# Kernel tuning notes

Hardware: AMD Instinct MI355X
Metric: run time of the kernel (lower is better)

Reference implementation:

```python
import jax, jax.numpy as jnp
import numpy as np

FRAME = 512
HOP = 256
FS = 16000
XI_H1 = 31.622776601683793
P_H0 = 0.5
P_H1 = 0.5
SMOOTH_T = 0.072
ALPHA = float(np.exp(-HOP / (FS * SMOOTH_T)))  # time_to_smoothing_constant
EPS = float(np.finfo(np.float32).eps)


def _sqrt_hann():
    # periodic Hann (torch.hann_window default), then sqrt (sqrt=True in STFTTorch)
    n = np.arange(FRAME)
    w = 0.5 * (1.0 - np.cos(2.0 * np.pi * n / FRAME))
    return jnp.asarray(np.sqrt(w), dtype=jnp.float32)


def _stft_power(x):
    # x: [B, N] time signal -> [B, F, T] power spectrogram (|STFT|^2)
    pad = FRAME // 2
    xp = jnp.pad(x, ((0, 0), (pad, pad)), mode='reflect')  # center=True, reflect
    T = (xp.shape[1] - FRAME) // HOP + 1
    idx = jnp.arange(T)[:, None] * HOP + jnp.arange(FRAME)[None, :]
    frames = xp[:, idx] * _sqrt_hann()          # [B, T, FRAME]
    spec = jnp.fft.rfft(frames, axis=-1)        # [B, T, F], F = FRAME//2 + 1
    power = spec.real ** 2 + spec.imag ** 2
    return jnp.transpose(power, (0, 2, 1)).astype(jnp.float32)  # [B, F, T]


def setup_inputs() -> dict:
    key = jax.random.key(0)
    k1, k2, k3 = jax.random.split(key, 3)
    B, N = 64, 128000
    F, T = FRAME // 2 + 1, N // HOP + 1  # 257, 501
    return {
        'spp_estimate': jax.random.uniform(k1, (B, 1, F, T), dtype=jnp.float32),
        'input_sig': jax.random.normal(k2, (B, 1, N), dtype=jnp.float32),
        'interference': jax.random.normal(k3, (B, 1, N), dtype=jnp.float32),
    }


def reference(spp_estimate, input_sig, interference):
    noise_p = _stft_power(interference[:, 0])   # [B, F, T]
    noisy_p = _stft_power(input_sig[:, 0])      # [B, F, T]

    # EMA noise-variance recursion over frames (sequential dependency)
    p = jnp.transpose(noise_p, (2, 0, 1))       # [T, B, F]

    def step(v, pt):
        v2 = ALPHA * v + (1.0 - ALPHA) * pt
        return v2, v2

    v0 = p[0]
    _, vs = jax.lax.scan(step, v0, p[1:])
    var_noise = jnp.concatenate([v0[None], vs], axis=0)  # [T, B, F]
    var_noise = jnp.transpose(var_noise, (1, 2, 0))      # [B, F, T]

    # a-posteriori SPP
    ratio = (P_H0 / P_H1) * (1.0 + XI_H1)
    expo = -noisy_p / (var_noise + EPS) * (XI_H1 / (1.0 + XI_H1))
    spp_oracle = 1.0 / (1.0 + ratio * jnp.exp(expo))

    est = spp_estimate[:, 0]                    # [B, F, T]
    loss = jnp.mean((est - spp_oracle) ** 2)
    return loss
```

## Files before the change

### kernel.cpp

```cpp
#include <hip/hip_runtime.h>
#include <hip/hip_bf16.h>
#include <math.h>

typedef __attribute__((ext_vector_type(8))) short bf16x8;
typedef __attribute__((ext_vector_type(4))) float f32x4;
typedef __attribute__((ext_vector_type(8))) _Float16 h8;
typedef unsigned long long u64;

#define NSAMP  128000
#define TFR    501
#define TP     512
#define FPOW   257
#define NF     257
#define B_SZ   64
#define CHUNKT 32
#define NCH    16
#define EPS_F  1.1920928955078125e-07f

#define SEG    16640
#define ASEGB  66560
#define BPHB   32768

__global__ __launch_bounds__(256)
void build_basis(unsigned short* __restrict__ Bt) {
    int col = blockIdx.x;
    int g = col >> 5, o = col & 15;
    int isIm = (col >> 4) & 1;
    int bin = g * 16 + o;
    for (int k = threadIdx.x; k < 512; k += 256) {
        float w = sinf((float)k * (float)(M_PI / 512.0));
        float v;
        if (col == 16) {
            v = w * ((k & 1) ? -1.f : 1.f);
        } else {
            int mm = (bin * k) & 511;
            float th = (float)mm * (float)(2.0 * M_PI / 512.0);
            v = w * (isIm ? -sinf(th) : cosf(th));
        }
        __hip_bfloat16 h = __float2bfloat16(v);
        int ph = k >> 5, kq = (k >> 3) & 3, j = k & 7;
        size_t idx = (((size_t)ph * 32 + (col >> 4)) * 64
                      + kq * 16 + (col & 15)) * 8 + j;
        Bt[idx] = *reinterpret_cast<unsigned short*>(&h);
    }
}

__global__ __launch_bounds__(512)
void dft_gemm(const float* __restrict__ sig,
              const float* __restrict__ intf,
              const unsigned short* __restrict__ Bt,
              _Float16* __restrict__ powo)
{
    extern __shared__ char As[];

    const int mchunk = blockIdx.x, b = blockIdx.y, s = blockIdx.z;
    const int tid = threadIdx.x, lane = tid & 63, wn = tid >> 6;
    const int lq = lane >> 4, ll = lane & 15;
    const float* x = (s == 0 ? intf : sig) + (size_t)b * NSAMP;
    const int tbase = mchunk * 16384 - 256;

    if (mchunk >= 1 && mchunk <= 6) {
        const char* xg = (const char*)(x + tbase);
        #pragma unroll
        for (int r = 0; r < 8; ++r) {
            int o = r * 8192 + tid * 16;
            __builtin_amdgcn_global_load_lds(
                (const __attribute__((address_space(1))) void*)(xg + o),
                (__attribute__((address_space(3))) void*)(As + o), 16, 0, 0);
        }
        if (tid < 64) {
            int o = 65536 + tid * 16;
            __builtin_amdgcn_global_load_lds(
                (const __attribute__((address_space(1))) void*)(xg + o),
                (__attribute__((address_space(3))) void*)(As + o), 16, 0, 0);
        }
    } else if (mchunk == 0) {
        const char* xg = (const char*)x;
        #pragma unroll
        for (int r = 0; r < 8; ++r) {
            int o = 1024 + r * 8192 + tid * 16;
            __builtin_amdgcn_global_load_lds(
                (const __attribute__((address_space(1))) void*)(xg + o - 1024),
                (__attribute__((address_space(3))) void*)(As + o), 16, 0, 0);
        }
    } else {
        const char* xg = (const char*)(x + tbase);
        #pragma unroll
        for (int r = 0; r < 6; ++r) {
            int o = r * 8192 + tid * 16;
            __builtin_amdgcn_global_load_lds(
                (const __attribute__((address_space(1))) void*)(xg + o),
                (__attribute__((address_space(3))) void*)(As + o), 16, 0, 0);
        }
        if (tid < 320) {
            int o = 49152 + tid * 16;
            __builtin_amdgcn_global_load_lds(
                (const __attribute__((address_space(1))) void*)(xg + o),
                (__attribute__((address_space(3))) void*)(As + o), 16, 0, 0);
        }
    }

    const char* bb = (const char*)Bt + (size_t)(wn * 4 * 64 + lane) * 16;
    bf16x8 B0[4], B1[4];
    auto loadPh = [&](int ph, bf16x8 (&dst)[4]) {
        const char* bp = bb + (size_t)ph * BPHB;
        #pragma unroll
        for (int nf = 0; nf < 4; ++nf)
            dst[nf] = *(const bf16x8*)(bp + nf * 1024);
    };
    loadPh(0, B0);

    asm volatile("s_waitcnt vmcnt(0)" ::: "memory");
    __syncthreads();

    if (mchunk == 0) {
        if (tid < 256) {
            float v = *(const float*)(As + (512 - tid) * 4);
            *(float*)(As + tid * 4) = v;
        }
        __syncthreads();
    } else if (mchunk == 7) {
        #pragma unroll
        for (int q = 0; q < 6; ++q) {
            int j = 13568 + q * 512 + tid;
            float v = *(const float*)(As + (27134 - j) * 4);
            *(float*)(As + j * 4) = v;
        }
        __syncthreads();
    }

    {
        float fr[32];
        float fx[4];
        #pragma unroll
        for (int q = 0; q < 8; ++q) {
            f32x4 v = *(const f32x4*)(As + (q * 512 + tid) * 16);
            fr[q*4+0] = v[0]; fr[q*4+1] = v[1];
            fr[q*4+2] = v[2]; fr[q*4+3] = v[3];
        }
        if (tid < 64) {
            f32x4 v = *(const f32x4*)(As + (4096 + tid) * 16);
            fx[0] = v[0]; fx[1] = v[1]; fx[2] = v[2]; fx[3] = v[3];
        }
        __syncthreads();
        #pragma unroll
        for (int q = 0; q < 8; ++q) {
            unsigned short h[4];
            #pragma unroll
            for (int e = 0; e < 4; ++e) {
                __hip_bfloat16 t = __float2bfloat16(fr[q*4+e]);
                h[e] = *(unsigned short*)&t;
            }
            int a = (q * 512 + tid) * 8;
            a ^= ((a >> 9) & 7) << 4;
            *(u64*)(As + a) = (u64)h[0] | ((u64)h[1] << 16) |
                              ((u64)h[2] << 32) | ((u64)h[3] << 48);
        }
        if (tid < 64) {
            unsigned short h[4];
            #pragma unroll
            for (int e = 0; e < 4; ++e) {
                __hip_bfloat16 t = __float2bfloat16(fx[e]);
                h[e] = *(unsigned short*)&t;
            }
            int a = (4096 + tid) * 8;
            *(u64*)(As + a) = (u64)h[0] | ((u64)h[1] << 16) |
                              ((u64)h[2] << 32) | ((u64)h[3] << 48);
        }
        __syncthreads();
    }

    f32x4 acc[4][4];
    #pragma unroll
    for (int i = 0; i < 4; ++i)
        #pragma unroll
        for (int j = 0; j < 4; ++j) acc[i][j] = 0;

    auto doPhase = [&](int ph, bf16x8 (&cur)[4]) {
        bf16x8 af[4];
        #pragma unroll
        for (int mf = 0; mf < 4; ++mf) {
            int a = (mf * 16 + ll) * 512 + ph * 64 + lq * 16;
            a ^= ((a >> 9) & 7) << 4;
            af[mf] = *(const bf16x8*)(As + a);
        }
        __builtin_amdgcn_s_setprio(1);
        #pragma unroll
        for (int mf = 0; mf < 4; ++mf)
            #pragma unroll
            for (int nf = 0; nf < 4; ++nf)
                acc[mf][nf] = __builtin_amdgcn_mfma_f32_16x16x32_bf16(
                    af[mf], cur[nf], acc[mf][nf], 0, 0, 0);
        __builtin_amdgcn_s_setprio(0);
    };

    #pragma unroll 1
    for (int pp2 = 0; pp2 < 8; ++pp2) {
        const int ph = pp2 * 2;
        loadPh(ph + 1, B1);
        doPhase(ph, B0);
        if (pp2 < 7) loadPh(ph + 2, B0);
        doPhase(ph + 1, B1);
    }

    const int sb = s * 64 + b;
    _Float16* pbase = powo + (size_t)sb * FPOW * TP;
    #pragma unroll
    for (int mf = 0; mf < 4; ++mf) {
        const int rl0 = mchunk * 64 + mf * 16 + lq * 4;
        #pragma unroll
        for (int p = 0; p < 2; ++p) {
            f32x4 re = acc[mf][2 * p], im = acc[mf][2 * p + 1];
            int gbin = wn * 2 + p;
            int bin = gbin * 16 + ll;
            bool nyq = (gbin == 0) && (ll == 0);
            unsigned short hp[4], hn[4];
            #pragma unroll
            for (int j = 0; j < 4; ++j) {
                float pr = re[j] * re[j];
                float pi = im[j] * im[j];
                _Float16 hv = (_Float16)(nyq ? pr : (pr + pi));
                hp[j] = *(unsigned short*)&hv;
                _Float16 hw = (_Float16)pi;
                hn[j] = *(unsigned short*)&hw;
            }
            u64 pk = (u64)hp[0] | ((u64)hp[1] << 16) |
                     ((u64)hp[2] << 32) | ((u64)hp[3] << 48);
            *(u64*)(pbase + (size_t)bin * TP + rl0) = pk;
            if (nyq) {
                u64 pk2 = (u64)hn[0] | ((u64)hn[1] << 16) |
                          ((u64)hn[2] << 32) | ((u64)hn[3] << 48);
                *(u64*)(pbase + (size_t)256 * TP + rl0) = pk2;
            }
        }
    }
}

template<int W>
__device__ __forceinline__ float warm_fixed(const _Float16* __restrict__ nrow,
                                            int base, float alpha, float oma) {
    h8 blk[W / 8];
    #pragma unroll
    for (int i = 0; i < W / 8; ++i)
        blk[i] = *(const h8*)(nrow + base + i * 8);
    float v = (float)blk[0][0];
    #pragma unroll
    for (int i = 1; i < W; ++i)
        v = fmaf(alpha, v, oma * (float)blk[i / 8][i % 8]);
    v = fmaf(alpha, v, oma * (float)nrow[base + W]);
    return v;
}

__global__ __launch_bounds__(256, 4)
void spp_loss_kernel(const _Float16* __restrict__ noiseP,
                     const _Float16* __restrict__ noisyP,
                     const float* __restrict__ est,
                     float* __restrict__ out,
                     float alpha)
{
    const double XI = 31.622776601683793;
    const float RATIO = (float)(1.0 + XI);
    const float COEF  = (float)(XI / (1.0 + XI));
    const float INVN  = (float)(1.0 / ((double)B_SZ * NF * TFR));

    int tid = blockIdx.x * blockDim.x + threadIdx.x;
    int f   = tid % NF;
    int rem = tid / NF;
    int c   = rem & (NCH - 1);
    int b   = rem >> 4;

    float local = 0.f;
    if (b < B_SZ) {
        const int t0   = c * CHUNKT;
        const int tend = min(TFR, t0 + CHUNKT);
        const _Float16* nrow = noiseP + ((size_t)b * NF + f) * TP;
        const _Float16* yrow = noisyP + ((size_t)b * NF + f) * TP;
        const float* erow = est + ((size_t)b * NF + f) * TFR;
        const float oma = 1.f - alpha;

        float v;
        if (t0 == 0)            v = (float)nrow[0];
        else if (t0 == CHUNKT)  v = warm_fixed<32>(nrow, 0, alpha, oma);
        else                    v = warm_fixed<48>(nrow, t0 - 48, alpha, oma);

        h8 wn8[4], wy8[4];
        #pragma unroll
        for (int i = 0; i < 4; ++i) {
            wn8[i] = *(const h8*)(nrow + t0 + i * 8);
            wy8[i] = *(const h8*)(yrow + t0 + i * 8);
        }
        float last_n = (float)nrow[t0 + 32];
        float last_y = (float)yrow[t0 + 32];
        float qe[32];
        #pragma unroll
        for (int i = 0; i < 32; ++i)
            qe[i] = erow[min(t0 + 1 + i, TFR - 1)];

        {
            float np = (float)wy8[0][0];
            float e0 = erow[t0];
            float expo = -np / (v + EPS_F) * COEF;
            float spp  = 1.f / fmaf(RATIO, __expf(expo), 1.f);
            float d = e0 - spp;
            local = fmaf(d, d, local);
        }
        #pragma unroll
        for (int i = 0; i < 32; ++i) {
            int t = t0 + 1 + i;
            float nv = (i < 31) ? (float)wn8[(i + 1) / 8][(i + 1) % 8] : last_n;
            v = fmaf(alpha, v, oma * nv);
            if (t < tend) {
                float yv = (i < 31) ? (float)wy8[(i + 1) / 8][(i + 1) % 8] : last_y;
                float expo = -yv / (v + EPS_F) * COEF;
                float spp  = 1.f / fmaf(RATIO, __expf(expo), 1.f);
                float d = qe[i] - spp;
                local = fmaf(d, d, local);
            }
        }
    }

    for (int off = 32; off > 0; off >>= 1)
        local += __shfl_down(local, off);
    __shared__ float wsum[4];
    if ((threadIdx.x & 63) == 0) wsum[threadIdx.x >> 6] = local;
    __syncthreads();
    if (threadIdx.x == 0) {
        float ssum = (wsum[0] + wsum[1]) + (wsum[2] + wsum[3]);
        atomicAdd(out, ssum * INVN);
    }
}

extern "C" void kernel_launch(void* const* d_in, const int* in_sizes, int n_in,
                              void* d_out, int out_size, void* d_ws, size_t ws_size,
                              hipStream_t stream) {
    const float* est  = (const float*)d_in[0];
    const float* sig  = (const float*)d_in[1];
    const float* intf = (const float*)d_in[2];

    unsigned short* Bt = (unsigned short*)d_ws;
    _Float16* powp = (_Float16*)((char*)d_ws + (size_t)512 * 1024);

    hipLaunchKernelGGL(build_basis, dim3(512), dim3(256), 0, stream, Bt);
    hipMemsetAsync(d_out, 0, sizeof(float), stream);

    hipFuncSetAttribute((const void*)dft_gemm,
                        hipFuncAttributeMaxDynamicSharedMemorySize, ASEGB);
    dim3 gG(8, 64, 2);
    hipLaunchKernelGGL(dft_gemm, gG, dim3(512), ASEGB, stream,
                       sig, intf, Bt, powp);

    const double alpha_d = exp(-((double)256) / (16000.0 * 0.072));
    const _Float16* noiseP = powp;
    const _Float16* noisyP = powp + (size_t)B_SZ * FPOW * TP;
    dim3 gB((B_SZ * NCH * NF + 255) / 256);
    hipLaunchKernelGGL(spp_loss_kernel, gB, dim3(256), 0, stream,
                       noiseP, noisyP, est, (float*)d_out, (float)alpha_d);
}
```

Measured before the change: 84.98 us.

## Split DFT into even/odd bins via folded windowed frames to halve GEMM K

Applies the sqrt-Hann window in the kernel and folds each 512-sample frame into sum and difference halves (x[m]±x[m+256]). Even bins then come from the sum half and odd bins from the difference half, so each wave group runs a K=256 GEMM instead of K=512. The basis is rebuilt as two 256-row groups, and a window table is staged in LDS. This halves the MFMA work and basis traffic, at the cost of extra LDS and some pre-processing arithmetic.

```diff
diff --git a/kernel.cpp b/kernel.cpp
--- a/kernel.cpp
+++ b/kernel.cpp
@@ -18,30 +18,36 @@
 #define EPS_F  1.1920928955078125e-07f
 
 #define SEG    16640
-#define ASEGB  66560
-#define BPHB   32768
+#define RAWB   66560
+#define WOFF   66560
+#define LDS_TOTAL 68608
+#define BGRPB  131072
+#define BPHB2  16384
 
 __global__ __launch_bounds__(256)
-void build_basis(unsigned short* __restrict__ Bt) {
-    int col = blockIdx.x;
-    int g = col >> 5, o = col & 15;
-    int isIm = (col >> 4) & 1;
-    int bin = g * 16 + o;
-    for (int k = threadIdx.x; k < 512; k += 256) {
-        float w = sinf((float)k * (float)(M_PI / 512.0));
-        float v;
-        if (col == 16) {
-            v = w * ((k & 1) ? -1.f : 1.f);
-        } else {
-            int mm = (bin * k) & 511;
-            float th = (float)mm * (float)(2.0 * M_PI / 512.0);
-            v = w * (isIm ? -sinf(th) : cosf(th));
-        }
-        __hip_bfloat16 h = __float2bfloat16(v);
-        int ph = k >> 5, kq = (k >> 3) & 3, j = k & 7;
-        size_t idx = (((size_t)ph * 32 + (col >> 4)) * 64
-                      + kq * 16 + (col & 15)) * 8 + j;
-        Bt[idx] = *reinterpret_cast<unsigned short*>(&h);
+void build_basis(unsigned short* __restrict__ Bt, float* __restrict__ wtab) {
+    const int c = blockIdx.x;
+    const int grp = c >> 8, cc = c & 255;
+    const int eo = (cc >> 5) * 16 + (cc & 15);
+    const int isIm = (cc >> 4) & 1;
+    const int bin = grp ? (2 * eo + 1) : (2 * eo);
+    const int m = threadIdx.x;
+    float v;
+    if (grp == 0 && cc == 16) {
+        v = (m & 1) ? -1.f : 1.f;
+    } else {
+        int mm = (bin * m) & 511;
+        float th = (float)mm * (float)(2.0 * M_PI / 512.0);
+        v = isIm ? -sinf(th) : cosf(th);
+    }
+    __hip_bfloat16 h = __float2bfloat16(v);
+    int ph = m >> 5, cg16 = cc >> 4;
+    int lane = ((m >> 3) & 3) * 16 + (cc & 15);
+    size_t idx = (((size_t)(grp * 8 + ph) * 16 + cg16) * 64 + lane) * 8 + (m & 7);
+    Bt[idx] = *reinterpret_cast<unsigned short*>(&h);
+    if (c == 0) {
+        wtab[m]       = sinf((float)m * (float)(M_PI / 512.0));
+        wtab[m + 256] = sinf((float)(m + 256) * (float)(M_PI / 512.0));
     }
 }
 
@@ -49,6 +55,7 @@
 void dft_gemm(const float* __restrict__ sig,
               const float* __restrict__ intf,
               const unsigned short* __restrict__ Bt,
+              const float* __restrict__ wtab,
               _Float16* __restrict__ powo)
 {
     extern __shared__ char As[];
@@ -99,11 +106,20 @@
                 (__attribute__((address_space(3))) void*)(As + o), 16, 0, 0);
         }
     }
-
-    const char* bb = (const char*)Bt + (size_t)(wn * 4 * 64 + lane) * 16;
+    if (tid < 128) {
+        int o = tid * 16;
+        __builtin_amdgcn_global_load_lds(
+            (const __attribute__((address_space(1))) void*)((const char*)wtab + o),
+            (__attribute__((address_space(3))) void*)(As + WOFF + o), 16, 0, 0);
+    }
+
+    const int grp = wn >> 2;
+    const int grpoff = grp * 512;
+    const char* WB = (const char*)Bt + (size_t)grp * BGRPB
+                   + (wn & 3) * 4096 + lane * 16;
     bf16x8 B0[4], B1[4];
     auto loadPh = [&](int ph, bf16x8 (&dst)[4]) {
-        const char* bp = bb + (size_t)ph * BPHB;
+        const char* bp = WB + (size_t)ph * BPHB2;
         #pragma unroll
         for (int nf = 0; nf < 4; ++nf)
             dst[nf] = *(const bf16x8*)(bp + nf * 1024);
@@ -130,42 +146,46 @@
     }
 
     {
-        float fr[32];
-        float fx[4];
-        #pragma unroll
-        for (int q = 0; q < 8; ++q) {
-            f32x4 v = *(const f32x4*)(As + (q * 512 + tid) * 16);
-            fr[q*4+0] = v[0]; fr[q*4+1] = v[1];
-            fr[q*4+2] = v[2]; fr[q*4+3] = v[3];
-        }
-        if (tid < 64) {
-            f32x4 v = *(const f32x4*)(As + (4096 + tid) * 16);
-            fx[0] = v[0]; fx[1] = v[1]; fx[2] = v[2]; fx[3] = v[3];
-        }
-        __syncthreads();
-        #pragma unroll
-        for (int q = 0; q < 8; ++q) {
-            unsigned short h[4];
+        const char* wt = As + WOFF;
+        #pragma unroll 1
+        for (int hh = 0; hh < 2; ++hh) {
+            f32x4 xa[4], xb[4];
             #pragma unroll
-            for (int e = 0; e < 4; ++e) {
-                __hip_bfloat16 t = __float2bfloat16(fr[q*4+e]);
-                h[e] = *(unsigned short*)&t;
-            }
-            int a = (q * 512 + tid) * 8;
-            a ^= ((a >> 9) & 7) << 4;
-            *(u64*)(As + a) = (u64)h[0] | ((u64)h[1] << 16) |
-                              ((u64)h[2] << 32) | ((u64)h[3] << 48);
-        }
-        if (tid < 64) {
-            unsigned short h[4];
+            for (int i = 0; i < 4; ++i) {
+                int qid = i * 512 + tid;
+                int row = hh * 32 + (qid >> 6);
+                int mq = qid & 63;
+                int ra = row * 1024 + mq * 16;
+                xa[i] = *(const f32x4*)(As + ra);
+                xb[i] = *(const f32x4*)(As + ra + 1024);
+            }
+            __syncthreads();
             #pragma unroll
-            for (int e = 0; e < 4; ++e) {
-                __hip_bfloat16 t = __float2bfloat16(fx[e]);
-                h[e] = *(unsigned short*)&t;
-            }
-            int a = (4096 + tid) * 8;
-            *(u64*)(As + a) = (u64)h[0] | ((u64)h[1] << 16) |
-                              ((u64)h[2] << 32) | ((u64)h[3] << 48);
+            for (int i = 0; i < 4; ++i) {
+                int qid = i * 512 + tid;
+                int row = hh * 32 + (qid >> 6);
+                int mq = qid & 63;
+                f32x4 we = *(const f32x4*)(wt + mq * 16);
+                f32x4 wo = *(const f32x4*)(wt + 1024 + mq * 16);
+                unsigned short he[4], ho[4];
+                #pragma unroll
+                for (int e = 0; e < 4; ++e) {
+                    float pa = xa[i][e] * we[e];
+                    float pb = xb[i][e] * wo[e];
+                    __hip_bfloat16 t0 = __float2bfloat16(pa + pb);
+                    __hip_bfloat16 t1 = __float2bfloat16(pa - pb);
+                    he[e] = *(unsigned short*)&t0;
+                    ho[e] = *(unsigned short*)&t1;
+                }
+                int ae = row * 1024 + mq * 8;
+                int ao = ae + 512;
+                ae ^= ((ae >> 10) & 7) << 4;
+                ao ^= ((ao >> 10) & 7) << 4;
+                *(u64*)(As + ae) = (u64)he[0] | ((u64)he[1] << 16) |
+                                   ((u64)he[2] << 32) | ((u64)he[3] << 48);
+                *(u64*)(As + ao) = (u64)ho[0] | ((u64)ho[1] << 16) |
+                                   ((u64)ho[2] << 32) | ((u64)ho[3] << 48);
+            }
         }
         __syncthreads();
     }
@@ -180,8 +200,8 @@
         bf16x8 af[4];
         #pragma unroll
         for (int mf = 0; mf < 4; ++mf) {
-            int a = (mf * 16 + ll) * 512 + ph * 64 + lq * 16;
-            a ^= ((a >> 9) & 7) << 4;
+            int a = (mf * 16 + ll) * 1024 + grpoff + ph * 64 + lq * 16;
+            a ^= ((a >> 10) & 7) << 4;
             af[mf] = *(const bf16x8*)(As + a);
         }
         __builtin_amdgcn_s_setprio(1);
@@ -195,11 +215,11 @@
     };
 
     #pragma unroll 1
-    for (int pp2 = 0; pp2 < 8; ++pp2) {
+    for (int pp2 = 0; pp2 < 4; ++pp2) {
         const int ph = pp2 * 2;
         loadPh(ph + 1, B1);
         doPhase(ph, B0);
-        if (pp2 < 7) loadPh(ph + 2, B0);
+        if (pp2 < 3) loadPh(ph + 2, B0);
         doPhase(ph + 1, B1);
     }
 
@@ -211,9 +231,10 @@
         #pragma unroll
         for (int p = 0; p < 2; ++p) {
             f32x4 re = acc[mf][2 * p], im = acc[mf][2 * p + 1];
-            int gbin = wn * 2 + p;
-            int bin = gbin * 16 + ll;
-            bool nyq = (gbin == 0) && (ll == 0);
+            int gb = (wn & 3) * 2 + p;
+            int eo = gb * 16 + ll;
+            int bin = grp ? (2 * eo + 1) : (2 * eo);
+            bool nyq = (grp == 0) && (gb == 0) && (ll == 0);
             unsigned short hp[4], hn[4];
             #pragma unroll
             for (int j = 0; j < 4; ++j) {
@@ -338,16 +359,17 @@
     const float* intf = (const float*)d_in[2];
 
     unsigned short* Bt = (unsigned short*)d_ws;
+    float* wtab = (float*)((char*)d_ws + (size_t)262144);
     _Float16* powp = (_Float16*)((char*)d_ws + (size_t)512 * 1024);
 
-    hipLaunchKernelGGL(build_basis, dim3(512), dim3(256), 0, stream, Bt);
+    hipLaunchKernelGGL(build_basis, dim3(512), dim3(256), 0, stream, Bt, wtab);
     hipMemsetAsync(d_out, 0, sizeof(float), stream);
 
     hipFuncSetAttribute((const void*)dft_gemm,
-                        hipFuncAttributeMaxDynamicSharedMemorySize, ASEGB);
+                        hipFuncAttributeMaxDynamicSharedMemorySize, LDS_TOTAL);
     dim3 gG(8, 64, 2);
-    hipLaunchKernelGGL(dft_gemm, gG, dim3(512), ASEGB, stream,
-                       sig, intf, Bt, powp);
+    hipLaunchKernelGGL(dft_gemm, gG, dim3(512), LDS_TOTAL, stream,
+                       sig, intf, Bt, wtab, powp);
 
     const double alpha_d = exp(-((double)256) / (16000.0 * 0.072));
     const _Float16* noiseP = powp;
```

Result: faster. 74.52 us (-12.3%).
